# Performance work log

Measured on AMD Instinct MI355X. Metric: run time of the kernel, lower is better.

## Reference

```python
import jax, jax.numpy as jnp
import numpy as np

EMBED_DIM = 256
NUM_CLASSES = 10


def setup_inputs() -> dict:
    key = jax.random.key(0)
    k1, k2, k3, k4 = jax.random.split(key, 4)
    x = jax.random.normal(k1, (64, 196, 768), dtype=jnp.float32)
    ag_w = jax.random.normal(k2, (EMBED_DIM, 768), dtype=jnp.float32)
    ag_b = jax.random.normal(k3, (EMBED_DIM,), dtype=jnp.float32)
    lm_w = jax.random.normal(k4, (EMBED_DIM * NUM_CLASSES, 768), dtype=jnp.float32)
    return {"x": x, "ag_w": ag_w, "ag_b": ag_b, "lm_w": lm_w}


def reference(x, ag_w, ag_b, lm_w):
    # x: (B, HW, D); ag_w: (E, D); ag_b: (E,); lm_w: (E*C, D)
    B, HW, D = x.shape
    E, C = EMBED_DIM, NUM_CLASSES
    # frozen arrangement generator -> binary sign pattern (B, HW, E)
    sign_patterns = (jnp.einsum('bhd,ed->bhe', x, ag_w) + ag_b > 0).astype(x.dtype)
    # linear map: (B, HW, E*C) -> (B, HW, E, C)
    z = jnp.einsum('bhd,pd->bhp', x, lm_w).reshape(B, HW, E, C)
    # masked reduction over HW and embed dims
    preds = jnp.einsum('bhp,bhpc->bc', sign_patterns, z) / HW
    return preds / E
```

## Files before the change

### kernel.cpp

```cpp
#include <hip/hip_runtime.h>

#define B_    64
#define HW_   196
#define HWP_  224
#define D_    768
#define E_    256
#define C_    10
#define MP_   (B_*HWP_)
#define K3K_  (E_*D_)
#define K3NB_ 256

typedef __bf16 bf16x8 __attribute__((ext_vector_type(8)));
typedef __bf16 bf16x4 __attribute__((ext_vector_type(4)));
typedef __bf16 bf16x2 __attribute__((ext_vector_type(2)));
typedef float  f32x4  __attribute__((ext_vector_type(4)));

__device__ __forceinline__ void gld_lds16(const void* g, void* l) {
  __builtin_amdgcn_global_load_lds((const __attribute__((address_space(1))) void*)g,
                                   (__attribute__((address_space(3))) void*)l, 16, 0, 0);
}

__global__ __launch_bounds__(256) void k0_prep(const float* __restrict__ w,
                                               __bf16* __restrict__ whi,
                                               __bf16* __restrict__ wlo,
                                               const float* __restrict__ lmw,
                                               __bf16* __restrict__ w2) {
  int bid = blockIdx.x;
  if (bid < 192) {
    size_t i4 = ((size_t)bid * 256 + threadIdx.x) * 4;
    float4 v = *(const float4*)&w[i4];
    float vv[4] = {v.x, v.y, v.z, v.w};
    bf16x4 h, l;
#pragma unroll
    for (int j = 0; j < 4; j++) {
      __bf16 hj = (__bf16)vv[j];
      float r = vv[j] - (float)hj;
      h[j] = hj;
      l[j] = (__bf16)r;
    }
    *(bf16x4*)&whi[i4] = h;
    *(bf16x4*)&wlo[i4] = l;
  } else {
    size_t i4 = ((size_t)(bid - 192) * 256 + threadIdx.x) * 4;
    int c = (int)(i4 / K3K_);
    int rem = (int)(i4 - (size_t)c * K3K_);
    int e = rem / D_;
    int d = rem - e * D_;
    bf16x4 o;
    if (c < C_) {
      float4 v = *(const float4*)&lmw[((size_t)e * C_ + c) * D_ + d];
      o[0] = (__bf16)v.x; o[1] = (__bf16)v.y; o[2] = (__bf16)v.z; o[3] = (__bf16)v.w;
    } else {
      o[0] = o[1] = o[2] = o[3] = (__bf16)0.0f;
    }
    *(bf16x4*)&w2[i4] = o;
  }
}

__global__ __launch_bounds__(256) void k1_signs(const float* __restrict__ x,
                                                const __bf16* __restrict__ whi,
                                                const __bf16* __restrict__ wlo,
                                                const float* __restrict__ bias,
                                                __bf16* __restrict__ st) {
  __shared__ __align__(16) char smem[36864];
  __bf16* Ah = (__bf16*)smem;
  __bf16* Al = (__bf16*)(smem + 10240);
  const int m0 = blockIdx.x * 64;
  const int tid = threadIdx.x;
  const int wave = tid >> 6, lane = tid & 63;
  const int wn = wave * 64;
  const int q = lane >> 4, l15 = lane & 15;

  const int ar = tid >> 2, ac = (tid & 3) * 8;
  const int am = m0 + ar;
  const int ab = am / HWP_;
  const int ahp = am - ab * HWP_;
  const bool avalid = (ahp < HW_);
  const float* aptr = &x[((size_t)ab * HW_ + (avalid ? ahp : 0)) * D_ + ac];

  const size_t boff = (size_t)(wn + l15) * D_ + q * 8;

  f32x4 acc[4][4] = {};
  float4 aX0, aX1, aY0, aY1;
  bf16x8 bh0[4], bl0[4], bh1[4], bl1[4];

#define K1_LOADA(r0, r1, kk) do { \
    r0 = *(const float4*)&aptr[(kk)]; \
    r1 = *(const float4*)&aptr[(kk) + 4]; \
  } while (0)

#define K1_CONV(buf, r0, r1) do { \
    float va[8] = {r0.x, r0.y, r0.z, r0.w, r1.x, r1.y, r1.z, r1.w}; \
    bf16x8 hh, ll; \
    _Pragma("unroll") \
    for (int j = 0; j < 8; j++) { \
      float vj = avalid ? va[j] : 0.0f; \
      __bf16 hj = (__bf16)vj; float rr = vj - (float)hj; \
      hh[j] = hj; ll[j] = (__bf16)rr; \
    } \
    *(bf16x8*)&Ah[(buf) * 2560 + ar * 40 + ac] = hh; \
    *(bf16x8*)&Al[(buf) * 2560 + ar * 40 + ac] = ll; \
  } while (0)

#define K1_LOADB(bh, bl, kk) do { \
    _Pragma("unroll") \
    for (int t = 0; t < 4; t++) { \
      bh[t] = *(const bf16x8*)&whi[boff + (size_t)t * 16 * D_ + (kk)]; \
      bl[t] = *(const bf16x8*)&wlo[boff + (size_t)t * 16 * D_ + (kk)]; \
    } \
  } while (0)

#define K1_BAR() do { \
    asm volatile("s_waitcnt lgkmcnt(0)" ::: "memory"); \
    __builtin_amdgcn_s_barrier(); \
    __builtin_amdgcn_sched_barrier(0); \
  } while (0)

#define K1_COMPUTE(buf, bh, bl) do { \
    bf16x8 ah[4], al[4]; \
    _Pragma("unroll") \
    for (int t = 0; t < 4; t++) { \
      int ra = (buf) * 2560 + (t * 16 + l15) * 40 + q * 8; \
      ah[t] = *(const bf16x8*)&Ah[ra]; \
      al[t] = *(const bf16x8*)&Al[ra]; \
    } \
    _Pragma("unroll") \
    for (int mt = 0; mt < 4; mt++) \
      _Pragma("unroll") \
      for (int nt = 0; nt < 4; nt++) { \
        acc[mt][nt] = __builtin_amdgcn_mfma_f32_16x16x32_bf16(ah[mt], bh[nt], acc[mt][nt], 0, 0, 0); \
        acc[mt][nt] = __builtin_amdgcn_mfma_f32_16x16x32_bf16(al[mt], bh[nt], acc[mt][nt], 0, 0, 0); \
        acc[mt][nt] = __builtin_amdgcn_mfma_f32_16x16x32_bf16(ah[mt], bl[nt], acc[mt][nt], 0, 0, 0); \
      } \
  } while (0)

  K1_LOADA(aX0, aX1, 0);
  K1_LOADB(bh0, bl0, 0);
  K1_LOADA(aY0, aY1, 32);
  K1_CONV(0, aX0, aX1);
  K1_BAR();

  for (int kb = 0; kb < 24; kb += 2) {
    K1_LOADB(bh1, bl1, (kb + 1) * 32);
    if (kb + 2 < 24) K1_LOADA(aX0, aX1, (kb + 2) * 32);
    K1_COMPUTE(0, bh0, bl0);
    K1_CONV(1, aY0, aY1);
    K1_BAR();
    if (kb + 2 < 24) K1_LOADB(bh0, bl0, (kb + 2) * 32);
    if (kb + 3 < 24) K1_LOADA(aY0, aY1, (kb + 3) * 32);
    K1_COMPUTE(1, bh1, bl1);
    if (kb + 2 < 24) K1_CONV(0, aX0, aX1);
    K1_BAR();
  }
#undef K1_LOADA
#undef K1_CONV
#undef K1_LOADB
#undef K1_BAR
#undef K1_COMPUTE

  __bf16* Sload = (__bf16*)smem;
#pragma unroll
  for (int mt = 0; mt < 4; mt++)
#pragma unroll
    for (int nt = 0; nt < 4; nt++) {
      int e = wn + nt * 16 + l15;
      float bv = bias[e];
      bf16x4 o;
#pragma unroll
      for (int r = 0; r < 4; r++) {
        int m = m0 + mt * 16 + q * 4 + r;
        int b = m / HWP_;
        int hp = m - b * HWP_;
        float v = acc[mt][nt][r] + bv;
        o[r] = (hp < HW_ && v > 0.0f) ? (__bf16)1.0f : (__bf16)0.0f;
      }
      *(bf16x4*)&Sload[e * 72 + mt * 16 + q * 4] = o;
    }
  __syncthreads();
#pragma unroll
  for (int it = 0; it < 16; it++) {
    int e = (tid >> 4) + it * 16;
    int m4 = (tid & 15) * 4;
    bf16x4 v = *(const bf16x4*)&Sload[e * 72 + m4];
    int mabs = m0 + m4;
    int b = mabs / HWP_;
    int hp = mabs - b * HWP_;
    *(bf16x4*)&st[((size_t)b * E_ + e) * HWP_ + hp] = v;
  }
}

__global__ __launch_bounds__(512) void k2_g(const __bf16* __restrict__ st,
                                            const float* __restrict__ x,
                                            __bf16* __restrict__ g) {
  __shared__ __align__(16) __bf16 As[2][256 * 32];
  __shared__ __align__(16) __bf16 Bs[2][128 * 40];
  const int f = blockIdx.x;
  const int xcd = f & 7;
  const int slot = f >> 3;
  const int b  = xcd + 8 * (slot / 6);
  const int d0 = (slot % 6) * 128;
  const int tid = threadIdx.x;
  const int wave = tid >> 6, lane = tid & 63;
  const int WE = (wave & 3) * 64;
  const int WD = (wave >> 2) * 64;
  const int q = lane >> 4, l15 = lane & 15;
  const int ar = tid >> 2, ac = (tid & 3) * 8;
  const int ldA = wave * 512;
  const int dg = tid & 31, kp = tid >> 5;
  f32x4 acc[4][4] = {};

  const __bf16* gA = &st[((size_t)b * E_ + ar) * HWP_ + ac];
  const float4 zero4 = make_float4(0.f, 0.f, 0.f, 0.f);
  float4 f0, f1;

#define K2_STAGEA(buf, kk) do { \
    gld_lds16(gA + (kk),                       &As[buf][ldA]); \
    gld_lds16(gA + (size_t)128 * HWP_ + (kk),  &As[buf][4096 + ldA]); \
  } while (0)

#define K2_LOADB(kk) do { \
    int hp0 = (kk) + 2 * kp; \
    const float* bsrc = &x[((size_t)b * HW_ + hp0) * D_ + d0 + 4 * dg]; \
    f0 = (hp0     < HW_) ? *(const float4*)&bsrc[0]  : zero4; \
    f1 = (hp0 + 1 < HW_) ? *(const float4*)&bsrc[D_] : zero4; \
  } while (0)

#define K2_WRITEB(buf) do { \
    float rr0[4] = {f0.x, f0.y, f0.z, f0.w}; \
    float rr1[4] = {f1.x, f1.y, f1.z, f1.w}; \
    _Pragma("unroll") \
    for (int j = 0; j < 4; j++) { \
      bf16x2 o; \
      o[0] = (__bf16)rr0[j]; o[1] = (__bf16)rr1[j]; \
      *(bf16x2*)&Bs[buf][(4 * dg + j) * 40 + 2 * kp] = o; \
    } \
  } while (0)

  K2_STAGEA(0, 0);
  K2_LOADB(0);
  K2_WRITEB(0);
  __syncthreads();

  int cur = 0;
  for (int k0 = 0; k0 < HWP_; k0 += 32) {
    const bool have = (k0 + 32 < HWP_);
    if (have) {
      K2_STAGEA(cur ^ 1, k0 + 32);
      K2_LOADB(k0 + 32);
    }
    bf16x8 af[4], bfr[4];
#pragma unroll
    for (int t = 0; t < 4; t++) {
      af[t]  = *(const bf16x8*)&As[cur][(WE + t * 16 + l15) * 32 + q * 8];
      bfr[t] = *(const bf16x8*)&Bs[cur][(WD + t * 16 + l15) * 40 + q * 8];
    }
#pragma unroll
    for (int mt = 0; mt < 4; mt++)
#pragma unroll
      for (int nt = 0; nt < 4; nt++)
        acc[mt][nt] = __builtin_amdgcn_mfma_f32_16x16x32_bf16(af[mt], bfr[nt], acc[mt][nt], 0, 0, 0);
    if (have) K2_WRITEB(cur ^ 1);
    __syncthreads();
    cur ^= 1;
  }
#undef K2_STAGEA
#undef K2_LOADB
#undef K2_WRITEB

#pragma unroll
  for (int mt = 0; mt < 4; mt++)
#pragma unroll
    for (int nt = 0; nt < 4; nt++) {
      int d = d0 + WD + nt * 16 + l15;
#pragma unroll
      for (int r = 0; r < 4; r++) {
        int e = WE + mt * 16 + q * 4 + r;
        g[((size_t)b * E_ + e) * D_ + d] = (__bf16)acc[mt][nt][r];
      }
    }
}

__global__ __launch_bounds__(256) void k3_mfma(const __bf16* __restrict__ g,
                                               const __bf16* __restrict__ w2,
                                               float* __restrict__ part) {
  __shared__ float sp[B_ * C_];
  const int tid = threadIdx.x;
  const int wave = tid >> 6, lane = tid & 63;
  const int q = lane >> 4, l15 = lane & 15;
  const int kbase = blockIdx.x * (K3K_ / K3NB_) + wave * (K3K_ / K3NB_ / 4);
  f32x4 acc[4] = {};

  for (int i = tid; i < B_ * C_; i += 256) sp[i] = 0.0f;

#pragma unroll
  for (int ks = 0; ks < 6; ks++) {
    int k = kbase + ks * 32 + q * 8;
    bf16x8 bfrag = *(const bf16x8*)&w2[(size_t)l15 * K3K_ + k];
#pragma unroll
    for (int mt = 0; mt < 4; mt++) {
      bf16x8 afrag = *(const bf16x8*)&g[(size_t)(mt * 16 + l15) * K3K_ + k];
      acc[mt] = __builtin_amdgcn_mfma_f32_16x16x32_bf16(afrag, bfrag, acc[mt], 0, 0, 0);
    }
  }
  __syncthreads();
  if (l15 < C_) {
#pragma unroll
    for (int mt = 0; mt < 4; mt++)
#pragma unroll
      for (int r = 0; r < 4; r++) {
        int b = mt * 16 + q * 4 + r;
        atomicAdd(&sp[b * C_ + l15], acc[mt][r]);
      }
  }
  __syncthreads();
  for (int i = tid; i < B_ * C_; i += 256)
    part[(size_t)blockIdx.x * (B_ * C_) + i] = sp[i];
}

__global__ __launch_bounds__(256) void k4_reduce(const float* __restrict__ part,
                                                 float* __restrict__ out) {
  __shared__ float sp[256];
  const int b = blockIdx.x;
  const int tid = threadIdx.x;
  const int c = tid & 15, g16 = tid >> 4;
  float s = 0.0f;
  if (c < C_) {
#pragma unroll
    for (int j = 0; j < 16; j++)
      s += part[(size_t)(g16 + 16 * j) * (B_ * C_) + b * C_ + c];
  }
  sp[tid] = s;
  __syncthreads();
  if (tid < C_) {
    float t = 0.0f;
#pragma unroll
    for (int j = 0; j < 16; j++) t += sp[j * 16 + tid];
    out[b * C_ + tid] = t * (1.0f / (196.0f * 256.0f));
  }
}

extern "C" void kernel_launch(void* const* d_in, const int* in_sizes, int n_in,
                              void* d_out, int out_size, void* d_ws, size_t ws_size,
                              hipStream_t stream) {
  const float* x    = (const float*)d_in[0];
  const float* ag_w = (const float*)d_in[1];
  const float* ag_b = (const float*)d_in[2];
  const float* lm_w = (const float*)d_in[3];
  float* out = (float*)d_out;

  char* ws = (char*)d_ws;
  const size_t W_BYTES  = (size_t)E_ * D_ * 2;
  const size_t ST_BYTES = (size_t)B_ * E_ * HWP_ * 2;
  const size_t G_BYTES  = (size_t)B_ * E_ * D_ * 2;
  const size_t W2_BYTES = (size_t)16 * K3K_ * 2;
  __bf16* whi  = (__bf16*)(ws);
  __bf16* wlo  = (__bf16*)(ws + W_BYTES);
  __bf16* st   = (__bf16*)(ws + 2 * W_BYTES);
  __bf16* gb   = (__bf16*)(ws + 2 * W_BYTES + ST_BYTES);
  __bf16* w2   = (__bf16*)(ws + 2 * W_BYTES + ST_BYTES + G_BYTES);
  float*  part = (float*)(ws + 2 * W_BYTES + ST_BYTES + G_BYTES + W2_BYTES);

  k0_prep<<<dim3(192 + (16 * K3K_) / 4 / 256), dim3(256), 0, stream>>>(ag_w, whi, wlo, lm_w, w2);
  k1_signs<<<dim3(MP_ / 64), dim3(256), 0, stream>>>(x, whi, wlo, ag_b, st);
  k2_g<<<dim3(6 * B_), dim3(512), 0, stream>>>(st, x, gb);
  k3_mfma<<<dim3(K3NB_), dim3(256), 0, stream>>>(gb, w2, part);
  k4_reduce<<<dim3(B_), dim3(256), 0, stream>>>(part, out);
}
```

Measured before the change: 154.5 us.

## Stage k1 weights in LDS via async DMA triple buffer; fuse lm_w conversion into k3

The sign-pattern GEMM now stages the hi/lo bf16 weight tiles into a triple-buffered LDS ring using global_load_lds, with XOR swizzling. It also raises wave priority around the MFMA blocks and unrolls the k-loop fully, replacing per-wave direct global register loads of B. Separately, k3 now reads lm_w in fp32 and converts it to bf16 inline, so k0 no longer writes a padded w2 buffer. This cuts a large prep pass and its memory traffic. The catch is that k1 now needs about 116 KB of LDS, which limits occupancy to one block per CU.

```diff
diff --git a/kernel.cpp b/kernel.cpp
--- a/kernel.cpp
+++ b/kernel.cpp
@@ -22,39 +22,20 @@
 
 __global__ __launch_bounds__(256) void k0_prep(const float* __restrict__ w,
                                                __bf16* __restrict__ whi,
-                                               __bf16* __restrict__ wlo,
-                                               const float* __restrict__ lmw,
-                                               __bf16* __restrict__ w2) {
-  int bid = blockIdx.x;
-  if (bid < 192) {
-    size_t i4 = ((size_t)bid * 256 + threadIdx.x) * 4;
-    float4 v = *(const float4*)&w[i4];
-    float vv[4] = {v.x, v.y, v.z, v.w};
-    bf16x4 h, l;
-#pragma unroll
-    for (int j = 0; j < 4; j++) {
-      __bf16 hj = (__bf16)vv[j];
-      float r = vv[j] - (float)hj;
-      h[j] = hj;
-      l[j] = (__bf16)r;
-    }
-    *(bf16x4*)&whi[i4] = h;
-    *(bf16x4*)&wlo[i4] = l;
-  } else {
-    size_t i4 = ((size_t)(bid - 192) * 256 + threadIdx.x) * 4;
-    int c = (int)(i4 / K3K_);
-    int rem = (int)(i4 - (size_t)c * K3K_);
-    int e = rem / D_;
-    int d = rem - e * D_;
-    bf16x4 o;
-    if (c < C_) {
-      float4 v = *(const float4*)&lmw[((size_t)e * C_ + c) * D_ + d];
-      o[0] = (__bf16)v.x; o[1] = (__bf16)v.y; o[2] = (__bf16)v.z; o[3] = (__bf16)v.w;
-    } else {
-      o[0] = o[1] = o[2] = o[3] = (__bf16)0.0f;
-    }
-    *(bf16x4*)&w2[i4] = o;
-  }
+                                               __bf16* __restrict__ wlo) {
+  size_t i4 = ((size_t)blockIdx.x * 256 + threadIdx.x) * 4;
+  float4 v = *(const float4*)&w[i4];
+  float vv[4] = {v.x, v.y, v.z, v.w};
+  bf16x4 h, l;
+#pragma unroll
+  for (int j = 0; j < 4; j++) {
+    __bf16 hj = (__bf16)vv[j];
+    float r = vv[j] - (float)hj;
+    h[j] = hj;
+    l[j] = (__bf16)r;
+  }
+  *(bf16x4*)&whi[i4] = h;
+  *(bf16x4*)&wlo[i4] = l;
 }
 
 __global__ __launch_bounds__(256) void k1_signs(const float* __restrict__ x,
@@ -62,14 +43,13 @@
                                                 const __bf16* __restrict__ wlo,
                                                 const float* __restrict__ bias,
                                                 __bf16* __restrict__ st) {
-  __shared__ __align__(16) char smem[36864];
-  __bf16* Ah = (__bf16*)smem;
-  __bf16* Al = (__bf16*)(smem + 10240);
+  __shared__ __align__(16) char smem[118784];
   const int m0 = blockIdx.x * 64;
   const int tid = threadIdx.x;
   const int wave = tid >> 6, lane = tid & 63;
   const int wn = wave * 64;
   const int q = lane >> 4, l15 = lane & 15;
+  const int swq = (q ^ ((l15 >> 1) & 3)) * 8;
 
   const int ar = tid >> 2, ac = (tid & 3) * 8;
   const int am = m0 + ar;
@@ -78,18 +58,20 @@
   const bool avalid = (ahp < HW_);
   const float* aptr = &x[((size_t)ab * HW_ + (avalid ? ahp : 0)) * D_ + ac];
 
-  const size_t boff = (size_t)(wn + l15) * D_ + q * 8;
+  const int swB = ((tid & 3) ^ ((tid >> 3) & 3)) * 8;
+  const size_t offB = (size_t)(tid >> 2) * D_ + swB;
 
   f32x4 acc[4][4] = {};
   float4 aX0, aX1, aY0, aY1;
-  bf16x8 bh0[4], bl0[4], bh1[4], bl1[4];
 
 #define K1_LOADA(r0, r1, kk) do { \
     r0 = *(const float4*)&aptr[(kk)]; \
     r1 = *(const float4*)&aptr[(kk) + 4]; \
   } while (0)
 
-#define K1_CONV(buf, r0, r1) do { \
+#define K1_CONV(bufA, r0, r1) do { \
+    __bf16* AhW = (__bf16*)(smem + 98304 + (bufA) * 10240); \
+    __bf16* AlW = AhW + 2560; \
     float va[8] = {r0.x, r0.y, r0.z, r0.w, r1.x, r1.y, r1.z, r1.w}; \
     bf16x8 hh, ll; \
     _Pragma("unroll") \
@@ -98,32 +80,35 @@
       __bf16 hj = (__bf16)vj; float rr = vj - (float)hj; \
       hh[j] = hj; ll[j] = (__bf16)rr; \
     } \
-    *(bf16x8*)&Ah[(buf) * 2560 + ar * 40 + ac] = hh; \
-    *(bf16x8*)&Al[(buf) * 2560 + ar * 40 + ac] = ll; \
-  } while (0)
-
-#define K1_LOADB(bh, bl, kk) do { \
+    *(bf16x8*)&AhW[ar * 40 + ac] = hh; \
+    *(bf16x8*)&AlW[ar * 40 + ac] = ll; \
+  } while (0)
+
+#define K1_DMAB(buf3, kk) do { \
+    char* bb = smem + (buf3) * 32768; \
+    _Pragma("unroll") \
+    for (int c = 0; c < 4; c++) { \
+      gld_lds16(&whi[offB + (size_t)c * 64 * D_ + (kk)], bb + c * 4096 + wave * 1024); \
+      gld_lds16(&wlo[offB + (size_t)c * 64 * D_ + (kk)], bb + 16384 + c * 4096 + wave * 1024); \
+    } \
+  } while (0)
+
+#define K1_COMPUTE(buf3, bufA) do { \
+    const __bf16* BhL = (const __bf16*)(smem + (buf3) * 32768); \
+    const __bf16* BlL = BhL + 8192; \
+    const __bf16* AhL = (const __bf16*)(smem + 98304 + (bufA) * 10240); \
+    const __bf16* AlL = AhL + 2560; \
+    bf16x8 ah[4], al[4], bh[4], bl[4]; \
     _Pragma("unroll") \
     for (int t = 0; t < 4; t++) { \
-      bh[t] = *(const bf16x8*)&whi[boff + (size_t)t * 16 * D_ + (kk)]; \
-      bl[t] = *(const bf16x8*)&wlo[boff + (size_t)t * 16 * D_ + (kk)]; \
+      int ra = (t * 16 + l15) * 40 + q * 8; \
+      int rb = (wn + t * 16 + l15) * 32 + swq; \
+      ah[t] = *(const bf16x8*)&AhL[ra]; \
+      al[t] = *(const bf16x8*)&AlL[ra]; \
+      bh[t] = *(const bf16x8*)&BhL[rb]; \
+      bl[t] = *(const bf16x8*)&BlL[rb]; \
     } \
-  } while (0)
-
-#define K1_BAR() do { \
-    asm volatile("s_waitcnt lgkmcnt(0)" ::: "memory"); \
-    __builtin_amdgcn_s_barrier(); \
-    __builtin_amdgcn_sched_barrier(0); \
-  } while (0)
-
-#define K1_COMPUTE(buf, bh, bl) do { \
-    bf16x8 ah[4], al[4]; \
-    _Pragma("unroll") \
-    for (int t = 0; t < 4; t++) { \
-      int ra = (buf) * 2560 + (t * 16 + l15) * 40 + q * 8; \
-      ah[t] = *(const bf16x8*)&Ah[ra]; \
-      al[t] = *(const bf16x8*)&Al[ra]; \
-    } \
+    __builtin_amdgcn_s_setprio(1); \
     _Pragma("unroll") \
     for (int mt = 0; mt < 4; mt++) \
       _Pragma("unroll") \
@@ -132,31 +117,47 @@
         acc[mt][nt] = __builtin_amdgcn_mfma_f32_16x16x32_bf16(al[mt], bh[nt], acc[mt][nt], 0, 0, 0); \
         acc[mt][nt] = __builtin_amdgcn_mfma_f32_16x16x32_bf16(ah[mt], bl[nt], acc[mt][nt], 0, 0, 0); \
       } \
-  } while (0)
-
+    __builtin_amdgcn_s_setprio(0); \
+  } while (0)
+
+#define K1_BAR() do { \
+    asm volatile("s_waitcnt lgkmcnt(0)" ::: "memory"); \
+    __builtin_amdgcn_s_barrier(); \
+    __builtin_amdgcn_sched_barrier(0); \
+  } while (0)
+
+  K1_DMAB(0, 0);
+  __builtin_amdgcn_sched_barrier(0);
   K1_LOADA(aX0, aX1, 0);
-  K1_LOADB(bh0, bl0, 0);
+  __builtin_amdgcn_sched_barrier(0);
+  K1_DMAB(1, 32);
+  __builtin_amdgcn_sched_barrier(0);
   K1_LOADA(aY0, aY1, 32);
   K1_CONV(0, aX0, aX1);
   K1_BAR();
 
-  for (int kb = 0; kb < 24; kb += 2) {
-    K1_LOADB(bh1, bl1, (kb + 1) * 32);
-    if (kb + 2 < 24) K1_LOADA(aX0, aX1, (kb + 2) * 32);
-    K1_COMPUTE(0, bh0, bl0);
-    K1_CONV(1, aY0, aY1);
+#pragma unroll
+  for (int t = 0; t < 22; ++t) {
+    K1_DMAB((t + 2) % 3, (t + 2) * 32);
+    __builtin_amdgcn_sched_barrier(0);
+    if ((t & 1) == 0) K1_LOADA(aX0, aX1, (t + 2) * 32);
+    else              K1_LOADA(aY0, aY1, (t + 2) * 32);
+    K1_COMPUTE(t % 3, t & 1);
+    if ((t & 1) == 0) K1_CONV(1, aY0, aY1);
+    else              K1_CONV(0, aX0, aX1);
     K1_BAR();
-    if (kb + 2 < 24) K1_LOADB(bh0, bl0, (kb + 2) * 32);
-    if (kb + 3 < 24) K1_LOADA(aY0, aY1, (kb + 3) * 32);
-    K1_COMPUTE(1, bh1, bl1);
-    if (kb + 2 < 24) K1_CONV(0, aX0, aX1);
-    K1_BAR();
-  }
+  }
+  K1_COMPUTE(22 % 3, 0);
+  K1_CONV(1, aY0, aY1);
+  K1_BAR();
+  K1_COMPUTE(23 % 3, 1);
+  K1_BAR();
+
 #undef K1_LOADA
 #undef K1_CONV
-#undef K1_LOADB
+#undef K1_DMAB
+#undef K1_COMPUTE
 #undef K1_BAR
-#undef K1_COMPUTE
 
   __bf16* Sload = (__bf16*)smem;
 #pragma unroll
@@ -281,21 +282,33 @@
 }
 
 __global__ __launch_bounds__(256) void k3_mfma(const __bf16* __restrict__ g,
-                                               const __bf16* __restrict__ w2,
+                                               const float* __restrict__ lmw,
                                                float* __restrict__ part) {
   __shared__ float sp[B_ * C_];
   const int tid = threadIdx.x;
   const int wave = tid >> 6, lane = tid & 63;
   const int q = lane >> 4, l15 = lane & 15;
-  const int kbase = blockIdx.x * (K3K_ / K3NB_) + wave * (K3K_ / K3NB_ / 4);
+  const int e = blockIdx.x;
   f32x4 acc[4] = {};
 
   for (int i = tid; i < B_ * C_; i += 256) sp[i] = 0.0f;
 
 #pragma unroll
   for (int ks = 0; ks < 6; ks++) {
-    int k = kbase + ks * 32 + q * 8;
-    bf16x8 bfrag = *(const bf16x8*)&w2[(size_t)l15 * K3K_ + k];
+    int d = wave * 192 + ks * 32 + q * 8;
+    size_t k = (size_t)e * D_ + d;
+    bf16x8 bfrag;
+    if (l15 < C_) {
+      const float* bp = &lmw[((size_t)e * C_ + l15) * D_ + d];
+      float4 b0 = *(const float4*)&bp[0];
+      float4 b1 = *(const float4*)&bp[4];
+      float bb[8] = {b0.x, b0.y, b0.z, b0.w, b1.x, b1.y, b1.z, b1.w};
+#pragma unroll
+      for (int j = 0; j < 8; j++) bfrag[j] = (__bf16)bb[j];
+    } else {
+#pragma unroll
+      for (int j = 0; j < 8; j++) bfrag[j] = (__bf16)0.0f;
+    }
 #pragma unroll
     for (int mt = 0; mt < 4; mt++) {
       bf16x8 afrag = *(const bf16x8*)&g[(size_t)(mt * 16 + l15) * K3K_ + k];
@@ -352,17 +365,15 @@
   const size_t W_BYTES  = (size_t)E_ * D_ * 2;
   const size_t ST_BYTES = (size_t)B_ * E_ * HWP_ * 2;
   const size_t G_BYTES  = (size_t)B_ * E_ * D_ * 2;
-  const size_t W2_BYTES = (size_t)16 * K3K_ * 2;
   __bf16* whi  = (__bf16*)(ws);
   __bf16* wlo  = (__bf16*)(ws + W_BYTES);
   __bf16* st   = (__bf16*)(ws + 2 * W_BYTES);
   __bf16* gb   = (__bf16*)(ws + 2 * W_BYTES + ST_BYTES);
-  __bf16* w2   = (__bf16*)(ws + 2 * W_BYTES + ST_BYTES + G_BYTES);
-  float*  part = (float*)(ws + 2 * W_BYTES + ST_BYTES + G_BYTES + W2_BYTES);
-
-  k0_prep<<<dim3(192 + (16 * K3K_) / 4 / 256), dim3(256), 0, stream>>>(ag_w, whi, wlo, lm_w, w2);
+  float*  part = (float*)(ws + 2 * W_BYTES + ST_BYTES + G_BYTES);
+
+  k0_prep<<<dim3(192), dim3(256), 0, stream>>>(ag_w, whi, wlo);
   k1_signs<<<dim3(MP_ / 64), dim3(256), 0, stream>>>(x, whi, wlo, ag_b, st);
   k2_g<<<dim3(6 * B_), dim3(512), 0, stream>>>(st, x, gb);
-  k3_mfma<<<dim3(K3NB_), dim3(256), 0, stream>>>(gb, w2, part);
+  k3_mfma<<<dim3(K3NB_), dim3(256), 0, stream>>>(gb, lm_w, part);
   k4_reduce<<<dim3(B_), dim3(256), 0, stream>>>(part, out);
 }
```

Result: faster. 148.1 us (-4.1%).
